# Kernel optimization log

Measured on AMD Instinct MI355X. Metric: run time of the kernel, lower is better.

Reference implementation:

```python
import jax, jax.numpy as jnp
import numpy as np

B, N, F_IN, F_OUT = 8, 2048, 128, 64
ALPHA = 0.2  # LeakyReLU negative slope
NEG_BIG = -9e15


def setup_inputs() -> dict:
    key = jax.random.key(0)
    k1, k2, k3, k4 = jax.random.split(key, 4)
    x = jax.random.normal(k1, (B, N, F_IN), dtype=jnp.float32)
    adj = jax.random.randint(k2, (B, N, N), 0, 2, dtype=jnp.int32)
    # xavier-uniform-ish init scale for faithfulness (gain=1.414)
    w_lim = 1.414 * np.sqrt(6.0 / (F_IN + F_OUT))
    a_lim = 1.414 * np.sqrt(6.0 / (2 * F_OUT + 1))
    weight = jax.random.uniform(k3, (F_IN, F_OUT), minval=-w_lim, maxval=w_lim, dtype=jnp.float32)
    weight2 = jax.random.uniform(k4, (2 * F_OUT, 1), minval=-a_lim, maxval=a_lim, dtype=jnp.float32)
    return {"x": x, "adj": adj, "weight": weight, "weight2": weight2}


def reference(x, adj, weight, weight2):
    # Linear projection: [B, N, F_out]
    wh = jnp.einsum("bnf,fo->bno", x, weight)
    # Additive GAT decomposition of concat-score:
    # e_ij = leakyrelu(a1 . Wh_i + a2 . Wh_j)  == original concat @ weight2
    a1 = weight2[:F_OUT, 0]   # [F_out]
    a2 = weight2[F_OUT:, 0]   # [F_out]
    s1 = wh @ a1              # [B, N]
    s2 = wh @ a2              # [B, N]
    e = s1[:, :, None] + s2[:, None, :]          # [B, N, N]
    e = jnp.where(e > 0, e, ALPHA * e)            # LeakyReLU
    e = jnp.where(adj > 0, e, NEG_BIG)            # mask non-edges
    attention = jax.nn.softmax(e, axis=2)         # [B, N, N]
    # dropout is identity in eval mode (training=False)
    out = jnp.einsum("bij,bjo->bio", attention, wh)  # [B, N, F_out]
    return jax.nn.elu(out)
```

## Files before the change

kernel.cpp:

```cpp
#include <hip/hip_runtime.h>
#include <cstdint>
#include <cstddef>

#define B_    8
#define N_    2048
#define FIN   128
#define FOUT  64
#define ALPHA 0.2f
#define NEG_BIG -9.0e15f

typedef __attribute__((ext_vector_type(8))) _Float16 half8;
typedef __attribute__((ext_vector_type(4))) float float4v;

__global__ __launch_bounds__(256, 4) void k1_wh(
    const float* __restrict__ x, const float* __restrict__ W,
    const float* __restrict__ w2, _Float16* __restrict__ whT,
    float* __restrict__ s1, float* __restrict__ s2)
{
    int t = threadIdx.x, lane = t & 63, w = t >> 6;
    float a1 = w2[lane], a2 = w2[FOUT + lane];
    int rowBase = blockIdx.x * 32 + w * 8;
    for (int rr = 0; rr < 8; ++rr) {
        int row = __builtin_amdgcn_readfirstlane(rowBase + rr);
        const float* xr = x + (size_t)row * FIN;
        float acc = 0.f;
        #pragma unroll
        for (int k = 0; k < FIN; ++k)
            acc = fmaf(xr[k], W[k * FOUT + lane], acc);
        int b = row >> 11, j = row & (N_ - 1);
        whT[((size_t)b * FOUT + lane) * N_ + j] = (_Float16)acc;
        float p1 = acc * a1, p2 = acc * a2;
        #pragma unroll
        for (int m = 32; m >= 1; m >>= 1) {
            p1 += __shfl_xor(p1, m);
            p2 += __shfl_xor(p2, m);
        }
        if (lane == 0) { s1[row] = p1; s2[row] = p2; }
    }
}

__global__ __launch_bounds__(256, 4) void k2_attn(
    const int* __restrict__ adj, const _Float16* __restrict__ whT,
    const float* __restrict__ s1, const float* __restrict__ s2,
    float* __restrict__ out)
{
    __shared__ __attribute__((aligned(16))) _Float16 pT[16][520];
    __shared__ float lL[16];
    __shared__ float smaxL[4];

    int t = threadIdx.x, lane = t & 63, w = t >> 6;
    int b = blockIdx.x >> 7;
    int i0 = (blockIdx.x & 127) << 4;

    const float4* s2v = (const float4*)(s2 + (size_t)b * N_);
    float4 ua = s2v[t], ub = s2v[t + 256];
    float vm = fmaxf(fmaxf(fmaxf(ua.x, ua.y), fmaxf(ua.z, ua.w)),
                     fmaxf(fmaxf(ub.x, ub.y), fmaxf(ub.z, ub.w)));
    #pragma unroll
    for (int m = 32; m >= 1; m >>= 1) vm = fmaxf(vm, __shfl_xor(vm, m));
    if (lane == 0) smaxL[w] = vm;
    __syncthreads();
    float s2max = fmaxf(fmaxf(smaxL[0], smaxL[1]), fmaxf(smaxL[2], smaxL[3]));

    int l15 = lane & 15, quad = lane >> 4;
    int f0 = w * 16;

    float s1r[4], negmh[4], lacc[4];
    #pragma unroll
    for (int rr = 0; rr < 4; ++rr) {
        float sv = s1[(size_t)b * N_ + i0 + w * 4 + rr];
        float mh = sv + s2max;
        mh = fmaxf(mh, ALPHA * mh);
        s1r[rr] = sv;
        negmh[rr] = -mh;
        lacc[rr] = 0.f;
    }

    float4v acc = {0, 0, 0, 0};
    const _Float16* wB = whT + ((size_t)b * FOUT + f0 + l15) * N_ + quad * 8;

    for (int jc = 0; jc < N_; jc += 512) {
        const float* s2c = s2 + (size_t)b * N_ + jc + lane * 8;
        float4 sa = *(const float4*)s2c;
        float4 sb = *(const float4*)(s2c + 4);
        float ss[8] = {sa.x, sa.y, sa.z, sa.w, sb.x, sb.y, sb.z, sb.w};

        #pragma unroll
        for (int rr = 0; rr < 4; ++rr) {
            int r = w * 4 + rr;
            const int* ap = adj + ((size_t)b * N_ + i0 + r) * N_ + jc + lane * 8;
            int4 aj0 = *(const int4*)ap;
            int4 aj1 = *(const int4*)(ap + 4);
            int aa[8] = {aj0.x, aj0.y, aj0.z, aj0.w, aj1.x, aj1.y, aj1.z, aj1.w};
            half8 pf;
            float ls = 0.f;
            #pragma unroll
            for (int e = 0; e < 8; ++e) {
                float v = s1r[rr] + ss[e];
                v = fmaxf(v, ALPHA * v);
                v = (aa[e] > 0) ? v : NEG_BIG;
                float tt = fmaxf(v + negmh[rr], -76.f);
                float p = __expf(tt);
                ls += p;
                pf[e] = (_Float16)p;
            }
            lacc[rr] += ls;
            *(half8*)&pT[r][lane * 8] = pf;
        }

        if (jc == N_ - 512) {
            #pragma unroll
            for (int rr = 0; rr < 4; ++rr) {
                float v = lacc[rr];
                #pragma unroll
                for (int m = 32; m >= 1; m >>= 1) v += __shfl_xor(v, m);
                if (lane == 0) lL[w * 4 + rr] = v;
            }
        }
        __syncthreads();

        const _Float16* wp = wB + jc;
        #pragma unroll
        for (int kk = 0; kk < 16; ++kk) {
            half8 af = *(const half8*)&pT[l15][kk * 32 + quad * 8];
            half8 bf = *(const half8*)(wp + kk * 32);
            acc = __builtin_amdgcn_mfma_f32_16x16x32_f16(af, bf, acc, 0, 0, 0);
        }
        __syncthreads();
    }

    #pragma unroll
    for (int reg = 0; reg < 4; ++reg) {
        int row = quad * 4 + reg;
        float val = acc[reg] / lL[row];
        val = (val > 0.f) ? val : (__expf(val) - 1.f);
        out[((size_t)b * N_ + i0 + row) * FOUT + f0 + l15] = val;
    }
}

extern "C" void kernel_launch(void* const* d_in, const int* in_sizes, int n_in,
                              void* d_out, int out_size, void* d_ws, size_t ws_size,
                              hipStream_t stream) {
    const float* x   = (const float*)d_in[0];
    const int*   adj = (const int*)d_in[1];
    const float* W   = (const float*)d_in[2];
    const float* w2  = (const float*)d_in[3];
    float* out = (float*)d_out;

    _Float16* whT = (_Float16*)d_ws;
    float* s1 = (float*)((char*)d_ws + (size_t)B_ * FOUT * N_ * 2);
    float* s2 = s1 + (size_t)B_ * N_;

    k1_wh<<<(B_ * N_) / 32, 256, 0, stream>>>(x, W, w2, whT, s1, s2);
    k2_attn<<<(B_ * N_) / 16, 256, 0, stream>>>(adj, whT, s1, s2, out);
}
```

Baseline: 254.3 us.

## Split attention key dimension across two blocks with atomic reduction and normalize pass

Each row-group's key range is split in half across two blocks, doubling the grid and raising the launch-bounds occupancy hint, with partial numerators and softmax denominators combined through float atomicAdd. A new normalization kernel then divides by the denominator and applies ELU. The aim is more parallelism and latency hiding on the bandwidth-bound adjacency stream. In exchange it adds two memsets, atomic traffic, an extra kernel launch, and an extra read/write of the output.

Result: slower. 286.2 us (+12.5%).

```diff
diff --git a/kernel.cpp b/kernel.cpp
--- a/kernel.cpp
+++ b/kernel.cpp
@@ -39,18 +39,20 @@
     }
 }
 
-__global__ __launch_bounds__(256, 4) void k2_attn(
+__global__ __launch_bounds__(256, 8) void k2_attn(
     const int* __restrict__ adj, const _Float16* __restrict__ whT,
     const float* __restrict__ s1, const float* __restrict__ s2,
-    float* __restrict__ out)
+    float* __restrict__ accP, float* __restrict__ lP)
 {
     __shared__ __attribute__((aligned(16))) _Float16 pT[16][520];
-    __shared__ float lL[16];
     __shared__ float smaxL[4];
 
     int t = threadIdx.x, lane = t & 63, w = t >> 6;
-    int b = blockIdx.x >> 7;
-    int i0 = (blockIdx.x & 127) << 4;
+    int rg = blockIdx.x >> 1;
+    int jh = blockIdx.x & 1;
+    int b = rg >> 7;
+    int i0 = (rg & 127) << 4;
+    int j0 = jh << 10;
 
     const float4* s2v = (const float4*)(s2 + (size_t)b * N_);
     float4 ua = s2v[t], ub = s2v[t + 256];
@@ -77,10 +79,10 @@
     }
 
     float4v acc = {0, 0, 0, 0};
-    const _Float16* wB = whT + ((size_t)b * FOUT + f0 + l15) * N_ + quad * 8;
+    const _Float16* wB = whT + ((size_t)b * FOUT + f0 + l15) * N_ + j0 + quad * 8;
 
-    for (int jc = 0; jc < N_; jc += 512) {
-        const float* s2c = s2 + (size_t)b * N_ + jc + lane * 8;
+    for (int jc = 0; jc < 1024; jc += 512) {
+        const float* s2c = s2 + (size_t)b * N_ + j0 + jc + lane * 8;
         float4 sa = *(const float4*)s2c;
         float4 sb = *(const float4*)(s2c + 4);
         float ss[8] = {sa.x, sa.y, sa.z, sa.w, sb.x, sb.y, sb.z, sb.w};
@@ -88,7 +90,7 @@
         #pragma unroll
         for (int rr = 0; rr < 4; ++rr) {
             int r = w * 4 + rr;
-            const int* ap = adj + ((size_t)b * N_ + i0 + r) * N_ + jc + lane * 8;
+            const int* ap = adj + ((size_t)b * N_ + i0 + r) * N_ + j0 + jc + lane * 8;
             int4 aj0 = *(const int4*)ap;
             int4 aj1 = *(const int4*)(ap + 4);
             int aa[8] = {aj0.x, aj0.y, aj0.z, aj0.w, aj1.x, aj1.y, aj1.z, aj1.w};
@@ -107,16 +109,6 @@
             lacc[rr] += ls;
             *(half8*)&pT[r][lane * 8] = pf;
         }
-
-        if (jc == N_ - 512) {
-            #pragma unroll
-            for (int rr = 0; rr < 4; ++rr) {
-                float v = lacc[rr];
-                #pragma unroll
-                for (int m = 32; m >= 1; m >>= 1) v += __shfl_xor(v, m);
-                if (lane == 0) lL[w * 4 + rr] = v;
-            }
-        }
         __syncthreads();
 
         const _Float16* wp = wB + jc;
@@ -130,12 +122,33 @@
     }
 
     #pragma unroll
+    for (int rr = 0; rr < 4; ++rr) {
+        float v = lacc[rr];
+        #pragma unroll
+        for (int m = 32; m >= 1; m >>= 1) v += __shfl_xor(v, m);
+        if (lane == 0) atomicAdd(&lP[(size_t)b * N_ + i0 + w * 4 + rr], v);
+    }
+    #pragma unroll
     for (int reg = 0; reg < 4; ++reg) {
         int row = quad * 4 + reg;
-        float val = acc[reg] / lL[row];
-        val = (val > 0.f) ? val : (__expf(val) - 1.f);
-        out[((size_t)b * N_ + i0 + row) * FOUT + f0 + l15] = val;
+        atomicAdd(&accP[((size_t)b * N_ + i0 + row) * FOUT + f0 + l15], acc[reg]);
     }
+}
+
+__global__ __launch_bounds__(256, 8) void k3_norm(
+    float* __restrict__ accP, const float* __restrict__ lP)
+{
+    int idx = blockIdx.x * 256 + threadIdx.x;
+    int row = idx >> 4;
+    float li = 1.0f / lP[row];
+    float4 v = ((const float4*)accP)[idx];
+    float r0 = v.x * li, r1 = v.y * li, r2 = v.z * li, r3 = v.w * li;
+    r0 = (r0 > 0.f) ? r0 : (__expf(r0) - 1.f);
+    r1 = (r1 > 0.f) ? r1 : (__expf(r1) - 1.f);
+    r2 = (r2 > 0.f) ? r2 : (__expf(r2) - 1.f);
+    r3 = (r3 > 0.f) ? r3 : (__expf(r3) - 1.f);
+    float4 o = {r0, r1, r2, r3};
+    ((float4*)accP)[idx] = o;
 }
 
 extern "C" void kernel_launch(void* const* d_in, const int* in_sizes, int n_in,
@@ -150,7 +163,12 @@
     _Float16* whT = (_Float16*)d_ws;
     float* s1 = (float*)((char*)d_ws + (size_t)B_ * FOUT * N_ * 2);
     float* s2 = s1 + (size_t)B_ * N_;
+    float* lP = s2 + (size_t)B_ * N_;
+
+    hipMemsetAsync(d_out, 0, (size_t)B_ * N_ * FOUT * sizeof(float), stream);
+    hipMemsetAsync(lP, 0, (size_t)B_ * N_ * sizeof(float), stream);
 
     k1_wh<<<(B_ * N_) / 32, 256, 0, stream>>>(x, W, w2, whT, s1, s2);
-    k2_attn<<<(B_ * N_) / 16, 256, 0, stream>>>(adj, whT, s1, s2, out);
+    k2_attn<<<(B_ * N_) / 16 * 2, 256, 0, stream>>>(adj, whT, s1, s2, out, lP);
+    k3_norm<<<(B_ * N_ * FOUT / 4) / 256, 256, 0, stream>>>(out, lP);
 }
```

## Pre-pack adjacency into bitmask and hoist s2 max into separate kernel

Applied to the files above, without the earlier changes.

Adds a pre-pass kernel that reads the int32 adjacency matrix and packs it into one bit per edge, so the attention kernel loads one byte of mask per 8 columns instead of 32 bytes of ints. The per-batch max of s2 moves into its own small kernel instead of being recomputed by every attention block. The attention kernel's launch bounds rise to 6 blocks per CU and its chunk loop is fully unrolled. The full adjacency read still happens once per call in the pack kernel, so the gain depends on the attention kernel having been latency-bound on those loads rather than bandwidth-bound. The change also adds two extra kernel launches and a round trip of the mask through global memory.

Result: slower. 304.3 us (+19.7%).

```diff
diff --git a/kernel.cpp b/kernel.cpp
--- a/kernel.cpp
+++ b/kernel.cpp
@@ -11,6 +11,28 @@
 
 typedef __attribute__((ext_vector_type(8))) _Float16 half8;
 typedef __attribute__((ext_vector_type(4))) float float4v;
+
+__global__ __launch_bounds__(256, 8) void k0_pack(
+    const int* __restrict__ adj, unsigned int* __restrict__ bm)
+{
+    int t = threadIdx.x, lane = t & 63, w = t >> 6;
+    int rowBase = blockIdx.x * 8 + w * 2;
+    #pragma unroll
+    for (int rr = 0; rr < 2; ++rr) {
+        int row = rowBase + rr;
+        const int* ap = adj + (size_t)row * N_ + lane * 32;
+        unsigned int m = 0;
+        #pragma unroll
+        for (int q = 0; q < 8; ++q) {
+            int4 a = *(const int4*)(ap + q * 4);
+            m |= (a.x > 0 ? 1u : 0u) << (q * 4 + 0);
+            m |= (a.y > 0 ? 1u : 0u) << (q * 4 + 1);
+            m |= (a.z > 0 ? 1u : 0u) << (q * 4 + 2);
+            m |= (a.w > 0 ? 1u : 0u) << (q * 4 + 3);
+        }
+        bm[(size_t)row * 64 + lane] = m;
+    }
+}
 
 __global__ __launch_bounds__(256, 4) void k1_wh(
     const float* __restrict__ x, const float* __restrict__ W,
@@ -39,28 +61,35 @@
     }
 }
 
-__global__ __launch_bounds__(256, 4) void k2_attn(
-    const int* __restrict__ adj, const _Float16* __restrict__ whT,
+__global__ void k1b_smax(const float* __restrict__ s2, float* __restrict__ smax)
+{
+    __shared__ float red[4];
+    int t = threadIdx.x, lane = t & 63, w = t >> 6;
+    const float4* p = (const float4*)(s2 + (size_t)blockIdx.x * N_);
+    float4 a = p[t], c = p[t + 256];
+    float m = fmaxf(fmaxf(fmaxf(a.x, a.y), fmaxf(a.z, a.w)),
+                    fmaxf(fmaxf(c.x, c.y), fmaxf(c.z, c.w)));
+    #pragma unroll
+    for (int s = 32; s >= 1; s >>= 1) m = fmaxf(m, __shfl_xor(m, s));
+    if (lane == 0) red[w] = m;
+    __syncthreads();
+    if (t == 0)
+        smax[blockIdx.x] = fmaxf(fmaxf(red[0], red[1]), fmaxf(red[2], red[3]));
+}
+
+__global__ __launch_bounds__(256, 6) void k2_attn(
+    const unsigned int* __restrict__ bm, const _Float16* __restrict__ whT,
     const float* __restrict__ s1, const float* __restrict__ s2,
-    float* __restrict__ out)
+    const float* __restrict__ smax, float* __restrict__ out)
 {
     __shared__ __attribute__((aligned(16))) _Float16 pT[16][520];
     __shared__ float lL[16];
-    __shared__ float smaxL[4];
 
     int t = threadIdx.x, lane = t & 63, w = t >> 6;
     int b = blockIdx.x >> 7;
     int i0 = (blockIdx.x & 127) << 4;
 
-    const float4* s2v = (const float4*)(s2 + (size_t)b * N_);
-    float4 ua = s2v[t], ub = s2v[t + 256];
-    float vm = fmaxf(fmaxf(fmaxf(ua.x, ua.y), fmaxf(ua.z, ua.w)),
-                     fmaxf(fmaxf(ub.x, ub.y), fmaxf(ub.z, ub.w)));
-    #pragma unroll
-    for (int m = 32; m >= 1; m >>= 1) vm = fmaxf(vm, __shfl_xor(vm, m));
-    if (lane == 0) smaxL[w] = vm;
-    __syncthreads();
-    float s2max = fmaxf(fmaxf(smaxL[0], smaxL[1]), fmaxf(smaxL[2], smaxL[3]));
+    float s2max = smax[b];
 
     int l15 = lane & 15, quad = lane >> 4;
     int f0 = w * 16;
@@ -76,39 +105,43 @@
         lacc[rr] = 0.f;
     }
 
+    const unsigned int* bmB =
+        bm + ((size_t)b * N_ + i0 + w * 4) * 64 + (lane >> 2);
+    int bsh = (lane & 3) * 8;
+    const float*    s2B = s2 + (size_t)b * N_ + lane * 8;
+    const _Float16* wB  = whT + ((size_t)b * FOUT + f0 + l15) * N_ + quad * 8;
+
     float4v acc = {0, 0, 0, 0};
-    const _Float16* wB = whT + ((size_t)b * FOUT + f0 + l15) * N_ + quad * 8;
 
-    for (int jc = 0; jc < N_; jc += 512) {
-        const float* s2c = s2 + (size_t)b * N_ + jc + lane * 8;
+    #pragma unroll
+    for (int c = 0; c < 4; ++c) {
+        const int jc = c * 512;
+
+        const float* s2c = s2B + jc;
         float4 sa = *(const float4*)s2c;
         float4 sb = *(const float4*)(s2c + 4);
         float ss[8] = {sa.x, sa.y, sa.z, sa.w, sb.x, sb.y, sb.z, sb.w};
 
         #pragma unroll
         for (int rr = 0; rr < 4; ++rr) {
-            int r = w * 4 + rr;
-            const int* ap = adj + ((size_t)b * N_ + i0 + r) * N_ + jc + lane * 8;
-            int4 aj0 = *(const int4*)ap;
-            int4 aj1 = *(const int4*)(ap + 4);
-            int aa[8] = {aj0.x, aj0.y, aj0.z, aj0.w, aj1.x, aj1.y, aj1.z, aj1.w};
+            unsigned int by = (bmB[(size_t)rr * 64 + c * 16] >> bsh) & 0xffu;
             half8 pf;
             float ls = 0.f;
             #pragma unroll
             for (int e = 0; e < 8; ++e) {
                 float v = s1r[rr] + ss[e];
                 v = fmaxf(v, ALPHA * v);
-                v = (aa[e] > 0) ? v : NEG_BIG;
+                v = (by & (1u << e)) ? v : NEG_BIG;
                 float tt = fmaxf(v + negmh[rr], -76.f);
                 float p = __expf(tt);
                 ls += p;
                 pf[e] = (_Float16)p;
             }
             lacc[rr] += ls;
-            *(half8*)&pT[r][lane * 8] = pf;
+            *(half8*)&pT[w * 4 + rr][lane * 8] = pf;
         }
 
-        if (jc == N_ - 512) {
+        if (c == 3) {
             #pragma unroll
             for (int rr = 0; rr < 4; ++rr) {
                 float v = lacc[rr];
@@ -147,10 +180,15 @@
     const float* w2  = (const float*)d_in[3];
     float* out = (float*)d_out;
 
-    _Float16* whT = (_Float16*)d_ws;
-    float* s1 = (float*)((char*)d_ws + (size_t)B_ * FOUT * N_ * 2);
-    float* s2 = s1 + (size_t)B_ * N_;
+    char* ws = (char*)d_ws;
+    _Float16*     whT  = (_Float16*)ws;                      ws += (size_t)B_ * FOUT * N_ * 2;
+    float*        s1   = (float*)ws;                         ws += (size_t)B_ * N_ * 4;
+    float*        s2   = (float*)ws;                         ws += (size_t)B_ * N_ * 4;
+    float*        smax = (float*)ws;                         ws += 256;
+    unsigned int* bmsk = (unsigned int*)ws;
 
+    k0_pack<<<(B_ * N_) / 8, 256, 0, stream>>>(adj, bmsk);
     k1_wh<<<(B_ * N_) / 32, 256, 0, stream>>>(x, W, w2, whT, s1, s2);
-    k2_attn<<<(B_ * N_) / 16, 256, 0, stream>>>(adj, whT, s1, s2, out);
+    k1b_smax<<<B_, 256, 0, stream>>>(s2, smax);
+    k2_attn<<<(B_ * N_) / 16, 256, 0, stream>>>(bmsk, whT, s1, s2, smax, out);
 }
```
